# Optimization experiments

Hardware: AMD Instinct MI355X
Metric: run time of the kernel (lower is better)

Reference implementation:

```python
import jax, jax.numpy as jnp
import numpy as np

SCALE = 10.0
THRESH = 1e-3   # nn.Threshold(eps, 0)
NORM_EPS = 1e-12  # F.normalize default eps
LEAKY_SLOPE = 0.01


def _proj(x, W1, W2):
    # x: [B, C, L]; conv1x1 == channel matmul
    h = jnp.einsum('oc,bcl->bol', W1, x)
    h = jnp.where(h >= 0, h, LEAKY_SLOPE * h)
    return jnp.einsum('oc,bcl->bol', W2, h)


def _l2norm(x):
    # normalize over channel dim (dim=1), torch F.normalize semantics
    n = jnp.sqrt(jnp.sum(x * x, axis=1, keepdims=True))
    return x / jnp.maximum(n, NORM_EPS)


def setup_inputs() -> dict:
    key = jax.random.key(0)
    k1, k2, k3, k4 = jax.random.split(key, 4)
    B, C, L, OUT = 4, 64, 4096, 64
    query = jax.random.normal(k1, (B, C, L), dtype=jnp.float32)
    kv = jax.random.normal(k2, (B, C, L), dtype=jnp.float32)
    W1 = jax.random.normal(k3, (2 * C, C), dtype=jnp.float32) * (1.0 / np.sqrt(C))
    W2 = jax.random.normal(k4, (OUT, 2 * C), dtype=jnp.float32) * (1.0 / np.sqrt(2 * C))
    return {"query": query, "key": kv, "W1": W1, "W2": W2}


def reference(query, key, W1, W2):
    # self_attention=True: query_conv is key_conv (shared weights)
    q = _l2norm(_proj(query, W1, W2))   # [B, O, L]
    k = _l2norm(_proj(key, W1, W2))     # [B, O, L]
    scores = jnp.einsum('bcl,bcm->blm', q, k) * SCALE  # [B, L, L]
    w = jax.nn.softmax(scores, axis=-1)
    return jnp.where(w > THRESH, w, 0.0)
```

## Files before the change

### kernel.cpp

```cpp
#include <hip/hip_runtime.h>
#include <math.h>

#define B 4
#define C 64
#define L 4096
#define OUTC 64
#define SCALE 10.0f
#define THRESH 1e-3f

typedef float v4f __attribute__((ext_vector_type(4)));
typedef short bf16x8 __attribute__((ext_vector_type(8)));
typedef unsigned short us8 __attribute__((ext_vector_type(8)));

__device__ __forceinline__ unsigned short f2bf(float x) {
    unsigned int u = __float_as_uint(x);
    u += 0x7fffu + ((u >> 16) & 1u);
    return (unsigned short)(u >> 16);
}
__device__ __forceinline__ float bf2f(unsigned short h) {
    return __uint_as_float(((unsigned int)h) << 16);
}
__device__ __forceinline__ v4f mfma16(bf16x8 a, bf16x8 b, v4f c) {
    return __builtin_amdgcn_mfma_f32_16x16x32_bf16(a, b, c, 0, 0, 0);
}


__global__ void __launch_bounds__(256) proj_kernel(
    const float* __restrict__ q_in, const float* __restrict__ k_in,
    const float* __restrict__ W1, const float* __restrict__ W2,
    unsigned short* __restrict__ Qh, unsigned short* __restrict__ Ql,
    unsigned short* __restrict__ Kh, unsigned short* __restrict__ Kl)
{
    int bid   = blockIdx.x;
    int xcd   = bid & 7;
    int b     = xcd >> 1;
    int which = (bid >> 3) & 1;
    int lt    = ((bid >> 4) << 1) | (xcd & 1);
    int l0    = lt << 6;
    int t     = threadIdx.x;
    int g     = t >> 6;
    int l     = t & 63;

    const float* __restrict__ src =
        (which ? k_in : q_in) + (size_t)b * C * L + l0 + l;
    unsigned short* __restrict__ dh = which ? Kh : Qh;
    unsigned short* __restrict__ dl = which ? Kl : Ql;

    __shared__ float Ht[128][65];
    __shared__ float red[4][64];

    float xr[C];
    #pragma unroll
    for (int c = 0; c < C; ++c)
        xr[c] = src[(size_t)c * L];

    #pragma unroll 1
    for (int oo = 0; oo < 32; oo += 4) {
        #pragma unroll
        for (int u = 0; u < 4; ++u) {
            int o = g * 32 + oo + u;
            float h0 = 0.f, h1 = 0.f, h2 = 0.f, h3 = 0.f;
            #pragma unroll
            for (int c = 0; c < C; c += 4) {
                h0 = fmaf(W1[o * C + c + 0], xr[c + 0], h0);
                h1 = fmaf(W1[o * C + c + 1], xr[c + 1], h1);
                h2 = fmaf(W1[o * C + c + 2], xr[c + 2], h2);
                h3 = fmaf(W1[o * C + c + 3], xr[c + 3], h3);
            }
            float h = (h0 + h1) + (h2 + h3);
            Ht[o][l] = (h >= 0.0f) ? h : 0.01f * h;
        }
    }
    __syncthreads();

    float y[16];
    #pragma unroll
    for (int u = 0; u < 16; ++u) y[u] = 0.f;

    #pragma unroll 1
    for (int hh = 0; hh < 2 * C; hh += 16) {
        float hr[16];
        #pragma unroll
        for (int r = 0; r < 16; ++r)
            hr[r] = Ht[hh + r][l];
        #pragma unroll
        for (int u = 0; u < 16; ++u) {
            int o = g * 16 + u;
            #pragma unroll
            for (int h = 0; h < 16; ++h)
                y[u] = fmaf(W2[o * (2 * C) + hh + h], hr[h], y[u]);
        }
    }

    float ss = 0.f;
    #pragma unroll
    for (int u = 0; u < 16; ++u) ss = fmaf(y[u], y[u], ss);
    red[g][l] = ss;
    __syncthreads();
    float tot = red[0][l] + red[1][l] + red[2][l] + red[3][l];
    float inv = 1.0f / fmaxf(sqrtf(tot), 1e-12f);

    unsigned short hs[16], ls[16];
    #pragma unroll
    for (int u = 0; u < 16; ++u) {
        float val = y[u] * inv;
        hs[u] = f2bf(val);
        ls[u] = f2bf(val - bf2f(hs[u]));
    }
    {
        int col   = l0 + l;
        int tile  = col >> 4;
        int lnn   = col & 15;
        int chunk = g >> 1;
        int quad0 = (g & 1) * 2;
        size_t base0 = (((size_t)b * 256 + tile) * 2 + chunk) * 512
                     + (size_t)(quad0 * 16 + lnn) * 8;
        size_t base1 = base0 + 128;
        *(us8*)(dh + base0) = *(us8*)&hs[0];
        *(us8*)(dh + base1) = *(us8*)&hs[8];
        *(us8*)(dl + base0) = *(us8*)&ls[0];
        *(us8*)(dl + base1) = *(us8*)&ls[8];
    }
}

__global__ void __launch_bounds__(512) scores_kernel(
    const unsigned short* __restrict__ Qh, const unsigned short* __restrict__ Ql,
    const unsigned short* __restrict__ Kh, const unsigned short* __restrict__ Kl,
    float* __restrict__ out)
{
    int bid  = blockIdx.x;
    int xcd  = bid & 7;
    int b    = xcd >> 1;
    int r0   = (((bid >> 3) << 1) | (xcd & 1)) << 5;
    int t    = threadIdx.x;
    int wave = t >> 6;
    int lane = t & 63;
    int quad = lane >> 4;
    int ln   = lane & 15;

    bf16x8 aQ[2][2][2];
    {
        #pragma unroll
        for (int rt = 0; rt < 2; ++rt) {
            size_t rowtile = (size_t)b * 256 + (r0 >> 4) + rt;
            #pragma unroll
            for (int c0 = 0; c0 < 2; ++c0) {
                size_t base = (rowtile * 2 + c0) * 512 + (size_t)lane * 8;
                aQ[rt][c0][0] = *(const bf16x8*)(Qh + base);
                aQ[rt][c0][1] = *(const bf16x8*)(Ql + base);
            }
        }
    }

    const size_t ktb = (size_t)b * 256;
    __shared__ float wsum[32][8];
    __shared__ float rinv[32];
    __shared__ float Pt[2][32][132];

    v4f ps[2];
    ps[0] = (v4f){0.f, 0.f, 0.f, 0.f};
    ps[1] = (v4f){0.f, 0.f, 0.f, 0.f};

    #pragma unroll 1
    for (int ct = 0; ct < 32; ++ct) {
        size_t base = ((ktb + wave * 32 + ct) * 2) * 512 + (size_t)lane * 8;
        bf16x8 bh0 = *(const bf16x8*)(Kh + base);
        bf16x8 bl0 = *(const bf16x8*)(Kl + base);
        bf16x8 bh1 = *(const bf16x8*)(Kh + base + 512);
        bf16x8 bl1 = *(const bf16x8*)(Kl + base + 512);

        #pragma unroll
        for (int rt = 0; rt < 2; ++rt) {
            v4f acc = (v4f){0.f, 0.f, 0.f, 0.f};
            acc = mfma16(aQ[rt][0][0], bh0, acc);
            acc = mfma16(aQ[rt][0][1], bh0, acc);
            acc = mfma16(aQ[rt][0][0], bl0, acc);
            acc = mfma16(aQ[rt][1][0], bh1, acc);
            acc = mfma16(aQ[rt][1][1], bh1, acc);
            acc = mfma16(aQ[rt][1][0], bl1, acc);
            #pragma unroll
            for (int r = 0; r < 4; ++r)
                ps[rt][r] += __expf(fmaf(SCALE, acc[r], -SCALE));
        }
    }

    #pragma unroll
    for (int rt = 0; rt < 2; ++rt) {
        #pragma unroll
        for (int r = 0; r < 4; ++r) {
            float s = ps[rt][r];
            s += __shfl_xor(s, 1);
            s += __shfl_xor(s, 2);
            s += __shfl_xor(s, 4);
            s += __shfl_xor(s, 8);
            if (ln == 0) wsum[rt * 16 + quad * 4 + r][wave] = s;
        }
    }
    __syncthreads();
    if (t < 32) {
        float s = 0.f;
        #pragma unroll
        for (int w = 0; w < 8; ++w) s += wsum[t][w];
        rinv[t] = 1.0f / s;
    }
    __syncthreads();

    float rv[2][4];
    #pragma unroll
    for (int rt = 0; rt < 2; ++rt)
        #pragma unroll
        for (int r = 0; r < 4; ++r)
            rv[rt][r] = rinv[rt * 16 + quad * 4 + r];

    float* __restrict__ outb = out + ((size_t)b * L + r0) * L;
    int srow = t >> 5;
    int scol = (t & 31) * 4;

    #pragma unroll 1
    for (int T = 0; T < 32; ++T) {
        int buf = T & 1;
        size_t base = ((ktb + T * 8 + wave) * 2) * 512 + (size_t)lane * 8;
        bf16x8 bh0 = *(const bf16x8*)(Kh + base);
        bf16x8 bl0 = *(const bf16x8*)(Kl + base);
        bf16x8 bh1 = *(const bf16x8*)(Kh + base + 512);
        bf16x8 bl1 = *(const bf16x8*)(Kl + base + 512);

        #pragma unroll
        for (int rt = 0; rt < 2; ++rt) {
            v4f acc = (v4f){0.f, 0.f, 0.f, 0.f};
            acc = mfma16(aQ[rt][0][0], bh0, acc);
            acc = mfma16(aQ[rt][0][1], bh0, acc);
            acc = mfma16(aQ[rt][0][0], bl0, acc);
            acc = mfma16(aQ[rt][1][0], bh1, acc);
            acc = mfma16(aQ[rt][1][1], bh1, acc);
            acc = mfma16(aQ[rt][1][0], bl1, acc);
            #pragma unroll
            for (int r = 0; r < 4; ++r) {
                float w = __expf(fmaf(SCALE, acc[r], -SCALE)) * rv[rt][r];
                w = (w > THRESH) ? w : 0.f;
                Pt[buf][rt * 16 + quad * 4 + r][wave * 16 + ln] = w;
            }
        }
        __syncthreads();

        #pragma unroll
        for (int j = 0; j < 2; ++j) {
            int row = j * 16 + srow;
            v4f o = *(const v4f*)&Pt[buf][row][scol];
            __builtin_nontemporal_store(
                o, (v4f*)(outb + (size_t)row * L + T * 128 + scol));
        }
    }
}

extern "C" void kernel_launch(void* const* d_in, const int* in_sizes, int n_in,
                              void* d_out, int out_size, void* d_ws, size_t ws_size,
                              hipStream_t stream) {
    const float* query = (const float*)d_in[0];
    const float* key   = (const float*)d_in[1];
    const float* W1    = (const float*)d_in[2];
    const float* W2    = (const float*)d_in[3];
    float* out = (float*)d_out;

    unsigned short* Qh = (unsigned short*)d_ws;
    unsigned short* Ql = Qh + (size_t)B * L * OUTC;
    unsigned short* Kh = Ql + (size_t)B * L * OUTC;
    unsigned short* Kl = Kh + (size_t)B * L * OUTC;

    hipLaunchKernelGGL(proj_kernel, dim3(512), dim3(256), 0, stream,
                       query, key, W1, W2, Qh, Ql, Kh, Kl);
    hipLaunchKernelGGL(scores_kernel, dim3(512), dim3(512), 0, stream,
                       Qh, Ql, Kh, Kl, out);
}
```

Before: 362.4 us.

## Cache first-pass exponentials in registers and halve rows per block

The scores kernel now stores each thread's exponentiated scores from the row-sum pass in a 32x4 register array and reuses them for the normalize/threshold/store pass. This removes the second set of K loads, MFMAs and exps. Each block now covers 16 rows instead of 32 and the grid doubles to keep the GPU filled. The large per-thread register array may raise VGPR usage and reduce occupancy, which risks spills or less latency hiding for the stores.

```diff
diff --git a/kernel.cpp b/kernel.cpp
--- a/kernel.cpp
+++ b/kernel.cpp
@@ -131,73 +131,66 @@
     int bid  = blockIdx.x;
     int xcd  = bid & 7;
     int b    = xcd >> 1;
-    int r0   = (((bid >> 3) << 1) | (xcd & 1)) << 5;
+    int r0   = (((bid >> 3) << 1) | (xcd & 1)) << 4;
     int t    = threadIdx.x;
     int wave = t >> 6;
     int lane = t & 63;
     int quad = lane >> 4;
     int ln   = lane & 15;
 
-    bf16x8 aQ[2][2][2];
+    bf16x8 aQ[2][2];
     {
-        #pragma unroll
-        for (int rt = 0; rt < 2; ++rt) {
-            size_t rowtile = (size_t)b * 256 + (r0 >> 4) + rt;
-            #pragma unroll
-            for (int c0 = 0; c0 < 2; ++c0) {
-                size_t base = (rowtile * 2 + c0) * 512 + (size_t)lane * 8;
-                aQ[rt][c0][0] = *(const bf16x8*)(Qh + base);
-                aQ[rt][c0][1] = *(const bf16x8*)(Ql + base);
-            }
+        size_t rowtile = (size_t)b * 256 + (r0 >> 4);
+        #pragma unroll
+        for (int c0 = 0; c0 < 2; ++c0) {
+            size_t base = (rowtile * 2 + c0) * 512 + (size_t)lane * 8;
+            aQ[c0][0] = *(const bf16x8*)(Qh + base);
+            aQ[c0][1] = *(const bf16x8*)(Ql + base);
         }
     }
 
     const size_t ktb = (size_t)b * 256;
-    __shared__ float wsum[32][8];
-    __shared__ float rinv[32];
-    __shared__ float Pt[2][32][132];
-
-    v4f ps[2];
-    ps[0] = (v4f){0.f, 0.f, 0.f, 0.f};
-    ps[1] = (v4f){0.f, 0.f, 0.f, 0.f};
-
-    #pragma unroll 1
-    for (int ct = 0; ct < 32; ++ct) {
-        size_t base = ((ktb + wave * 32 + ct) * 2) * 512 + (size_t)lane * 8;
+    __shared__ float wsum[16][8];
+    __shared__ float rinv[16];
+    __shared__ float Pt[2][16][132];
+
+    float e[32][4];
+    v4f ps = (v4f){0.f, 0.f, 0.f, 0.f};
+
+    #pragma unroll
+    for (int i = 0; i < 32; ++i) {
+        size_t base = ((ktb + i * 8 + wave) * 2) * 512 + (size_t)lane * 8;
         bf16x8 bh0 = *(const bf16x8*)(Kh + base);
         bf16x8 bl0 = *(const bf16x8*)(Kl + base);
         bf16x8 bh1 = *(const bf16x8*)(Kh + base + 512);
         bf16x8 bl1 = *(const bf16x8*)(Kl + base + 512);
 
-        #pragma unroll
-        for (int rt = 0; rt < 2; ++rt) {
-            v4f acc = (v4f){0.f, 0.f, 0.f, 0.f};
-            acc = mfma16(aQ[rt][0][0], bh0, acc);
-            acc = mfma16(aQ[rt][0][1], bh0, acc);
-            acc = mfma16(aQ[rt][0][0], bl0, acc);
-            acc = mfma16(aQ[rt][1][0], bh1, acc);
-            acc = mfma16(aQ[rt][1][1], bh1, acc);
-            acc = mfma16(aQ[rt][1][0], bl1, acc);
-            #pragma unroll
-            for (int r = 0; r < 4; ++r)
-                ps[rt][r] += __expf(fmaf(SCALE, acc[r], -SCALE));
-        }
-    }
-
-    #pragma unroll
-    for (int rt = 0; rt < 2; ++rt) {
+        v4f acc = (v4f){0.f, 0.f, 0.f, 0.f};
+        acc = mfma16(aQ[0][0], bh0, acc);
+        acc = mfma16(aQ[0][1], bh0, acc);
+        acc = mfma16(aQ[0][0], bl0, acc);
+        acc = mfma16(aQ[1][0], bh1, acc);
+        acc = mfma16(aQ[1][1], bh1, acc);
+        acc = mfma16(aQ[1][0], bl1, acc);
         #pragma unroll
         for (int r = 0; r < 4; ++r) {
-            float s = ps[rt][r];
-            s += __shfl_xor(s, 1);
-            s += __shfl_xor(s, 2);
-            s += __shfl_xor(s, 4);
-            s += __shfl_xor(s, 8);
-            if (ln == 0) wsum[rt * 16 + quad * 4 + r][wave] = s;
-        }
-    }
-    __syncthreads();
-    if (t < 32) {
+            float ev = __expf(fmaf(SCALE, acc[r], -SCALE));
+            e[i][r] = ev;
+            ps[r] += ev;
+        }
+    }
+
+    #pragma unroll
+    for (int r = 0; r < 4; ++r) {
+        float s = ps[r];
+        s += __shfl_xor(s, 1);
+        s += __shfl_xor(s, 2);
+        s += __shfl_xor(s, 4);
+        s += __shfl_xor(s, 8);
+        if (ln == 0) wsum[quad * 4 + r][wave] = s;
+    }
+    __syncthreads();
+    if (t < 16) {
         float s = 0.f;
         #pragma unroll
         for (int w = 0; w < 8; ++w) s += wsum[t][w];
@@ -205,51 +198,29 @@
     }
     __syncthreads();
 
-    float rv[2][4];
-    #pragma unroll
-    for (int rt = 0; rt < 2; ++rt)
-        #pragma unroll
-        for (int r = 0; r < 4; ++r)
-            rv[rt][r] = rinv[rt * 16 + quad * 4 + r];
+    float rv[4];
+    #pragma unroll
+    for (int r = 0; r < 4; ++r)
+        rv[r] = rinv[quad * 4 + r];
 
     float* __restrict__ outb = out + ((size_t)b * L + r0) * L;
     int srow = t >> 5;
     int scol = (t & 31) * 4;
 
-    #pragma unroll 1
+    #pragma unroll
     for (int T = 0; T < 32; ++T) {
         int buf = T & 1;
-        size_t base = ((ktb + T * 8 + wave) * 2) * 512 + (size_t)lane * 8;
-        bf16x8 bh0 = *(const bf16x8*)(Kh + base);
-        bf16x8 bl0 = *(const bf16x8*)(Kl + base);
-        bf16x8 bh1 = *(const bf16x8*)(Kh + base + 512);
-        bf16x8 bl1 = *(const bf16x8*)(Kl + base + 512);
-
-        #pragma unroll
-        for (int rt = 0; rt < 2; ++rt) {
-            v4f acc = (v4f){0.f, 0.f, 0.f, 0.f};
-            acc = mfma16(aQ[rt][0][0], bh0, acc);
-            acc = mfma16(aQ[rt][0][1], bh0, acc);
-            acc = mfma16(aQ[rt][0][0], bl0, acc);
-            acc = mfma16(aQ[rt][1][0], bh1, acc);
-            acc = mfma16(aQ[rt][1][1], bh1, acc);
-            acc = mfma16(aQ[rt][1][0], bl1, acc);
-            #pragma unroll
-            for (int r = 0; r < 4; ++r) {
-                float w = __expf(fmaf(SCALE, acc[r], -SCALE)) * rv[rt][r];
-                w = (w > THRESH) ? w : 0.f;
-                Pt[buf][rt * 16 + quad * 4 + r][wave * 16 + ln] = w;
-            }
+        #pragma unroll
+        for (int r = 0; r < 4; ++r) {
+            float w = e[T][r] * rv[r];
+            w = (w > THRESH) ? w : 0.f;
+            Pt[buf][quad * 4 + r][wave * 16 + ln] = w;
         }
         __syncthreads();
 
-        #pragma unroll
-        for (int j = 0; j < 2; ++j) {
-            int row = j * 16 + srow;
-            v4f o = *(const v4f*)&Pt[buf][row][scol];
-            __builtin_nontemporal_store(
-                o, (v4f*)(outb + (size_t)row * L + T * 128 + scol));
-        }
+        v4f o = *(const v4f*)&Pt[buf][srow][scol];
+        __builtin_nontemporal_store(
+            o, (v4f*)(outb + (size_t)srow * L + T * 128 + scol));
     }
 }
 
@@ -269,6 +240,6 @@
 
     hipLaunchKernelGGL(proj_kernel, dim3(512), dim3(256), 0, stream,
                        query, key, W1, W2, Qh, Ql, Kh, Kl);
-    hipLaunchKernelGGL(scores_kernel, dim3(512), dim3(512), 0, stream,
+    hipLaunchKernelGGL(scores_kernel, dim3(1024), dim3(512), 0, stream,
                        Qh, Ql, Kh, Kl, out);
 }
```

Measured after the change: 382.5 us. 1.06x slower.
